# Optimization experiments

Hardware: AMD Instinct MI355X
Metric: run time of the kernel (lower is better)

The kernel has to match this reference:

```python
import jax, jax.numpy as jnp
import numpy as np

EPS = 1e-12  # matches torch.nn.functional.normalize eps


def _normalize(x):
    n = jnp.sqrt(jnp.sum(x * x, axis=-1, keepdims=True))
    return x / jnp.maximum(n, EPS)


def setup_inputs() -> dict:
    key = jax.random.key(0)
    k1, k2, k3 = jax.random.split(key, 3)
    B, C, D = 1024, 32768, 512
    embeddings = jax.random.normal(k1, (B, D), dtype=jnp.float32)
    proxies = jax.random.normal(k2, (C, D), dtype=jnp.float32) / 8.0
    labels = jax.random.randint(k3, (B,), 0, C, dtype=jnp.int64)
    return {"embeddings": embeddings, "proxies": proxies, "labels": labels}


def reference(embeddings, proxies, labels):
    # batch: [B, D], P: [C, D], both scaled to norm 3
    batch = 3.0 * _normalize(embeddings)
    P = 3.0 * _normalize(proxies)

    # Squared euclidean distances to ALL proxies via the expansion
    # ||b - p||^2 = ||b||^2 + ||p||^2 - 2 b.p  -> [B, C]
    b_sq = jnp.sum(batch * batch, axis=-1, keepdims=True)      # [B, 1]
    p_sq = jnp.sum(P * P, axis=-1)                             # [C]
    dist = b_sq + p_sq[None, :] - 2.0 * (batch @ P.T)          # [B, C]

    B = batch.shape[0]
    rows = jnp.arange(B)
    pos_dist = dist[rows, labels]                              # [B]

    # logsumexp over negatives: mask out the positive class per row
    neg_scores = jnp.where(
        jnp.arange(dist.shape[1])[None, :] == labels[:, None],
        -jnp.inf,
        -dist,
    )
    neg_lse = jax.nn.logsumexp(neg_scores, axis=1)             # [B]

    return jnp.mean(pos_dist + neg_lse)
```

## Files before the change

### kernel.cpp

```cpp
#include <hip/hip_runtime.h>
#include <hip/hip_fp8.h>
#include <stdint.h>

#define D_DIM 512
#define B_ROWS 1024
#define C_ROWS 32768
#define NBLK (C_ROWS / 128)

typedef __attribute__((ext_vector_type(4))) float floatx4;
typedef __attribute__((ext_vector_type(4))) int intx4;
typedef __attribute__((ext_vector_type(8))) int intx8;

#define GLOBAL_AS __attribute__((address_space(1)))
#define LDS_AS __attribute__((address_space(3)))

__device__ inline void async_copy16(const unsigned char* g, unsigned char* l) {
    __builtin_amdgcn_global_load_lds((const GLOBAL_AS void*)g, (LDS_AS void*)l, 16, 0, 0);
}

__device__ inline unsigned char f2fp8(float x) {
    __hip_fp8_e4m3 t(x);
    return t.__x;
}
__device__ inline float fp8tof(unsigned char v) {
    __hip_fp8_e4m3 t;
    t.__x = v;
    return (float)t;
}


__global__ void norm_rows_kernel(const float* __restrict__ prox,
                                 const float* __restrict__ emb,
                                 unsigned char* __restrict__ Pq,
                                 unsigned char* __restrict__ Aq,
                                 float* __restrict__ acc,
                                 unsigned* __restrict__ ticket) {
    if (blockIdx.x == 0 && threadIdx.x == 0) { *acc = 0.f; *ticket = 0u; }
    const int wid = threadIdx.x >> 6;
    const int lane = threadIdx.x & 63;
    int row = blockIdx.x * 4 + wid;
    const float* src;
    unsigned char* dst;
    if (row < C_ROWS) {
        src = prox; dst = Pq;
    } else {
        row -= C_ROWS;
        src = emb; dst = Aq;
    }

    const float4* p = (const float4*)(src + (size_t)row * D_DIM + lane * 8);
    float4 v0 = p[0];
    float4 v1 = p[1];
    float ss = v0.x * v0.x + v0.y * v0.y + v0.z * v0.z + v0.w * v0.w +
               v1.x * v1.x + v1.y * v1.y + v1.z * v1.z + v1.w * v1.w;
#pragma unroll
    for (int off = 1; off < 64; off <<= 1) ss += __shfl_xor(ss, off);
    const float s = 3.0f * rsqrtf(ss);

    unsigned char q[8];
    q[0] = f2fp8(v0.x * s); q[1] = f2fp8(v0.y * s);
    q[2] = f2fp8(v0.z * s); q[3] = f2fp8(v0.w * s);
    q[4] = f2fp8(v1.x * s); q[5] = f2fp8(v1.y * s);
    q[6] = f2fp8(v1.z * s); q[7] = f2fp8(v1.w * s);
    uint2 packed;
    packed.x = (unsigned)q[0] | ((unsigned)q[1] << 8) |
               ((unsigned)q[2] << 16) | ((unsigned)q[3] << 24);
    packed.y = (unsigned)q[4] | ((unsigned)q[5] << 8) |
               ((unsigned)q[6] << 16) | ((unsigned)q[7] << 24);

    const size_t addr = (size_t)(row >> 4) * 8192 + (lane >> 4) * 2048 +
                        ((lane >> 1) & 1) * 1024 + ((lane >> 2) & 3) * 256 +
                        (row & 15) * 16 + (lane & 1) * 8;
    *(uint2*)(dst + addr) = packed;
}

__global__ void __launch_bounds__(256, 3)
gemm_lse_kernel(const unsigned char* __restrict__ Aq,
                const unsigned char* __restrict__ Bq,
                float* __restrict__ part) {
    __shared__ __align__(16) unsigned char sA[16384];
    __shared__ __align__(16) unsigned char sB[16384];
    __shared__ float red[128];

    const int tid = threadIdx.x;
    const int wid = tid >> 6;
    const int lane = tid & 63;
    const int n0t = blockIdx.x * 8;
    const int m0t = blockIdx.y * 8;

    if (tid < 128) red[tid] = 0.f;

    const int wmt = (wid >> 1) * 4;
    const int wnt = (wid & 1) * 4;
    const int wm = wmt * 16;
    const int fr = lane & 15;
    const int quad = lane >> 4;

    floatx4 acc[4][4];
    const floatx4 zero = {0.f, 0.f, 0.f, 0.f};
#pragma unroll
    for (int i = 0; i < 4; ++i)
#pragma unroll
        for (int j = 0; j < 4; ++j) acc[i][j] = zero;

    for (int c = 0; c < 4; ++c) {
#pragma unroll
        for (int j = 0; j < 4; ++j) {
            const int tl = wid * 2 + (j >> 1);
            const int half = j & 1;
            const size_t goA = (size_t)(m0t + tl) * 8192 + c * 2048 + half * 1024;
            const size_t goB = (size_t)(n0t + tl) * 8192 + c * 2048 + half * 1024;
            const int lo = tl * 2048 + half * 1024 + lane * 16;
            async_copy16(Aq + goA + lane * 16, &sA[lo]);
            async_copy16(Bq + goB + lane * 16, &sB[lo]);
        }
        __syncthreads();

        intx8 a8[4], b8[4];
#pragma unroll
        for (int t = 0; t < 4; ++t) {
            const int oa = (wmt + t) * 2048 + lane * 16;
            const int ob = (wnt + t) * 2048 + lane * 16;
            intx4 alo = *(const intx4*)&sA[oa];
            intx4 ahi = *(const intx4*)&sA[oa + 1024];
            intx4 blo = *(const intx4*)&sB[ob];
            intx4 bhi = *(const intx4*)&sB[ob + 1024];
            a8[t] = __builtin_shufflevector(alo, ahi, 0, 1, 2, 3, 4, 5, 6, 7);
            b8[t] = __builtin_shufflevector(blo, bhi, 0, 1, 2, 3, 4, 5, 6, 7);
        }
#pragma unroll
        for (int ti = 0; ti < 4; ++ti)
#pragma unroll
            for (int tj = 0; tj < 4; ++tj)
                acc[ti][tj] = __builtin_amdgcn_mfma_scale_f32_16x16x128_f8f6f4(
                    a8[ti], b8[tj], acc[ti][tj],
                    0 , 0 ,
                    0, 0x7F , 0, 0x7F );
        __syncthreads();
    }

#pragma unroll
    for (int ti = 0; ti < 4; ++ti) {
        float rs[4] = {0.f, 0.f, 0.f, 0.f};
#pragma unroll
        for (int tj = 0; tj < 4; ++tj)
#pragma unroll
            for (int r = 0; r < 4; ++r)
                rs[r] += __expf(2.0f * acc[ti][tj][r]);
#pragma unroll
        for (int r = 0; r < 4; ++r) {
            rs[r] += __shfl_xor(rs[r], 1);
            rs[r] += __shfl_xor(rs[r], 2);
            rs[r] += __shfl_xor(rs[r], 4);
            rs[r] += __shfl_xor(rs[r], 8);
        }
        if (fr == 0) {
#pragma unroll
            for (int r = 0; r < 4; ++r)
                atomicAdd(&red[wm + ti * 16 + quad * 4 + r], rs[r]);
        }
    }
    __syncthreads();
    if (tid < 128)
        part[(size_t)blockIdx.x * B_ROWS + m0t * 16 + tid] = red[tid];
}

__global__ void finalize_kernel(const float* __restrict__ part,
                                const unsigned char* __restrict__ Aq,
                                const unsigned char* __restrict__ Pq,
                                const int* __restrict__ labels,
                                float* __restrict__ acc,
                                unsigned* __restrict__ ticket,
                                float* __restrict__ out) {
    __shared__ float r4s[4];
    const int tid = threadIdx.x;
    const int wid = tid >> 6;
    const int lane = tid & 63;
    const int b = blockIdx.x * 4 + wid;

    float s = 0.f;
#pragma unroll
    for (int k = 0; k < 4; ++k)
        s += part[(size_t)(lane * 4 + k) * B_ROWS + b];

    const int l = labels[b];
    const size_t ua_addr = (size_t)(b >> 4) * 8192 + (lane >> 4) * 2048 +
                           ((lane >> 1) & 1) * 1024 + ((lane >> 2) & 3) * 256 +
                           (b & 15) * 16 + (lane & 1) * 8;
    const size_t ub_addr = (size_t)(l >> 4) * 8192 + (lane >> 4) * 2048 +
                           ((lane >> 1) & 1) * 1024 + ((lane >> 2) & 3) * 256 +
                           (l & 15) * 16 + (lane & 1) * 8;
    uint2 ua = *(const uint2*)(Aq + ua_addr);
    uint2 ub = *(const uint2*)(Pq + ub_addr);
    const unsigned char* au = (const unsigned char*)&ua;
    const unsigned char* bu = (const unsigned char*)&ub;
    float d = 0.f;
#pragma unroll
    for (int j = 0; j < 8; ++j) d += fp8tof(au[j]) * fp8tof(bu[j]);
#pragma unroll
    for (int off = 1; off < 64; off <<= 1) {
        s += __shfl_xor(s, off);
        d += __shfl_xor(d, off);
    }

    if (lane == 0) {
        float p2 = 2.0f * d;
        r4s[wid] = logf(s - __expf(p2)) - p2;
    }
    __syncthreads();
    if (tid == 0) {
        float bl = r4s[0] + r4s[1] + r4s[2] + r4s[3];
        atomicAdd(acc, bl);
        __threadfence();
        unsigned t = atomicAdd(ticket, 1u);
        if (t == 255u) {
            float total = atomicAdd(acc, 0.f);
            out[0] = total / (float)B_ROWS;
        }
    }
}

extern "C" void kernel_launch(void* const* d_in, const int* in_sizes, int n_in,
                              void* d_out, int out_size, void* d_ws, size_t ws_size,
                              hipStream_t stream) {
    const float* emb = (const float*)d_in[0];
    const float* prox = (const float*)d_in[1];
    const int* labels = (const int*)d_in[2];
    float* out = (float*)d_out;

    char* ws = (char*)d_ws;
    unsigned char* Pq = (unsigned char*)ws;
    unsigned char* Aq = Pq + (size_t)C_ROWS * D_DIM;
    float* part = (float*)(Aq + (size_t)B_ROWS * D_DIM);
    float* acc = part + (size_t)NBLK * B_ROWS;
    unsigned* ticket = (unsigned*)(acc + 1);

    norm_rows_kernel<<<(C_ROWS + B_ROWS) / 4, 256, 0, stream>>>(
        prox, emb, Pq, Aq, acc, ticket);
    gemm_lse_kernel<<<dim3(NBLK, B_ROWS / 128), 256, 0, stream>>>(Aq, Pq, part);
    finalize_kernel<<<B_ROWS / 4, 256, 0, stream>>>(
        part, Aq, Pq, labels, acc, ticket, out);
}
```

Measured before the change: 136.9 us.

## Double-buffer B tiles in LDS and load A fragments directly to registers

The FP8 GEMM kernel now keeps two LDS buffers for the proxy (B) chunk and prefetches the next K-chunk of B asynchronously while MFMAs run on the current one. The A operand no longer goes through LDS; each wave reads its A fragments straight from global memory into a double-buffered register array. The point is to overlap global loads with compute and to drop one barrier per K iteration. In exchange, two waves now load the same A rows redundantly, and register pressure rises from holding two sets of A fragments.

```diff
diff --git a/kernel.cpp b/kernel.cpp
--- a/kernel.cpp
+++ b/kernel.cpp
@@ -78,8 +78,7 @@
 gemm_lse_kernel(const unsigned char* __restrict__ Aq,
                 const unsigned char* __restrict__ Bq,
                 float* __restrict__ part) {
-    __shared__ __align__(16) unsigned char sA[16384];
-    __shared__ __align__(16) unsigned char sB[16384];
+    __shared__ __align__(16) unsigned char sB[2][16384];
     __shared__ float red[128];
 
     const int tid = threadIdx.x;
@@ -96,6 +95,8 @@
     const int fr = lane & 15;
     const int quad = lane >> 4;
 
+    const unsigned char* Abase = Aq + (size_t)(m0t + wmt) * 8192 + lane * 16;
+
     floatx4 acc[4][4];
     const floatx4 zero = {0.f, 0.f, 0.f, 0.f};
 #pragma unroll
@@ -103,41 +104,56 @@
 #pragma unroll
         for (int j = 0; j < 4; ++j) acc[i][j] = zero;
 
+#define STAGE_B(d, c)                                                         \
+    do {                                                                      \
+        _Pragma("unroll")                                                     \
+        for (int j = 0; j < 4; ++j) {                                         \
+            const int tl = wid * 2 + (j >> 1);                                \
+            const int half = j & 1;                                           \
+            async_copy16(Bq + (size_t)(n0t + tl) * 8192 + (c) * 2048 +        \
+                             half * 1024 + lane * 16,                         \
+                         &sB[d][tl * 2048 + half * 1024 + lane * 16]);        \
+        }                                                                     \
+    } while (0)
+
+    intx8 a[2][4];
+#define LOAD_A(d, c)                                                          \
+    do {                                                                      \
+        _Pragma("unroll")                                                     \
+        for (int t = 0; t < 4; ++t) {                                         \
+            intx4 lo = *(const intx4*)(Abase + t * 8192 + (c) * 2048);        \
+            intx4 hi = *(const intx4*)(Abase + t * 8192 + (c) * 2048 + 1024); \
+            a[d][t] = __builtin_shufflevector(lo, hi, 0, 1, 2, 3, 4, 5, 6, 7);\
+        }                                                                     \
+    } while (0)
+
+    STAGE_B(0, 0);
+    LOAD_A(0, 0);
+
+#pragma unroll
     for (int c = 0; c < 4; ++c) {
-#pragma unroll
-        for (int j = 0; j < 4; ++j) {
-            const int tl = wid * 2 + (j >> 1);
-            const int half = j & 1;
-            const size_t goA = (size_t)(m0t + tl) * 8192 + c * 2048 + half * 1024;
-            const size_t goB = (size_t)(n0t + tl) * 8192 + c * 2048 + half * 1024;
-            const int lo = tl * 2048 + half * 1024 + lane * 16;
-            async_copy16(Aq + goA + lane * 16, &sA[lo]);
-            async_copy16(Bq + goB + lane * 16, &sB[lo]);
-        }
+        const int cur = c & 1;
         __syncthreads();
-
-        intx8 a8[4], b8[4];
-#pragma unroll
-        for (int t = 0; t < 4; ++t) {
-            const int oa = (wmt + t) * 2048 + lane * 16;
-            const int ob = (wnt + t) * 2048 + lane * 16;
-            intx4 alo = *(const intx4*)&sA[oa];
-            intx4 ahi = *(const intx4*)&sA[oa + 1024];
-            intx4 blo = *(const intx4*)&sB[ob];
-            intx4 bhi = *(const intx4*)&sB[ob + 1024];
-            a8[t] = __builtin_shufflevector(alo, ahi, 0, 1, 2, 3, 4, 5, 6, 7);
-            b8[t] = __builtin_shufflevector(blo, bhi, 0, 1, 2, 3, 4, 5, 6, 7);
-        }
-#pragma unroll
-        for (int ti = 0; ti < 4; ++ti)
-#pragma unroll
-            for (int tj = 0; tj < 4; ++tj)
+        if (c < 3) {
+            STAGE_B(cur ^ 1, c + 1);
+            LOAD_A(cur ^ 1, c + 1);
+        }
+#pragma unroll
+        for (int tj = 0; tj < 4; ++tj) {
+            const int ob = (wnt + tj) * 2048 + lane * 16;
+            intx4 blo = *(const intx4*)&sB[cur][ob];
+            intx4 bhi = *(const intx4*)&sB[cur][ob + 1024];
+            intx8 b8 = __builtin_shufflevector(blo, bhi, 0, 1, 2, 3, 4, 5, 6, 7);
+#pragma unroll
+            for (int ti = 0; ti < 4; ++ti)
                 acc[ti][tj] = __builtin_amdgcn_mfma_scale_f32_16x16x128_f8f6f4(
-                    a8[ti], b8[tj], acc[ti][tj],
+                    a[cur][ti], b8, acc[ti][tj],
                     0 , 0 ,
                     0, 0x7F , 0, 0x7F );
-        __syncthreads();
-    }
+        }
+    }
+#undef STAGE_B
+#undef LOAD_A
 
 #pragma unroll
     for (int ti = 0; ti < 4; ++ti) {
```

New measurement: 143.5 us. 4.8% more time.
